# Kernel tuning notes

Hardware: AMD Instinct MI355X
Metric: run time of the kernel (lower is better)

The kernel has to match this reference:

```python
import jax, jax.numpy as jnp
import numpy as np

B, S, D, H = 2, 2048, 1024, 16
DK = D // H


def setup_inputs() -> dict:
    key = jax.random.key(0)
    ks = jax.random.split(key, 12)
    sc = 1.0 / np.sqrt(D)
    return {
        "q": jax.random.normal(ks[0], (B, S, D), jnp.float32),
        "k": jax.random.normal(ks[1], (B, S, D), jnp.float32),
        "v": jax.random.normal(ks[2], (B, S, D), jnp.float32),
        "mask": jax.random.randint(ks[3], (B, S), 0, 2, jnp.int32),
        "Wq": jax.random.normal(ks[4], (D, D), jnp.float32) * sc,
        "bq": jnp.zeros((D,), jnp.float32),
        "Wk": jax.random.normal(ks[5], (D, D), jnp.float32) * sc,
        "bk": jnp.zeros((D,), jnp.float32),
        "Wv": jax.random.normal(ks[6], (D, D), jnp.float32) * sc,
        "bv": jnp.zeros((D,), jnp.float32),
        "Wo": jax.random.normal(ks[7], (D, D), jnp.float32) * sc,
        "bo": jnp.zeros((D,), jnp.float32),
    }


def reference(q, k, v, mask, Wq, bq, Wk, bk, Wv, bv, Wo, bo):
    # Projections (flax nn.Dense: x @ W + b)
    query = q @ Wq + bq          # [B,S,D]
    key_ = k @ Wk + bk
    value = v @ Wv + bv
    # split heads -> [B,H,S,DK]
    def split(x):
        return x.reshape(B, S, H, DK).transpose(0, 2, 1, 3)
    qh, kh, vh = split(query), split(key_), split(value)
    scores = jnp.einsum('bhqd,bhkd->bhqk', qh, kh) / jnp.sqrt(jnp.float32(DK))
    # Faithful to source: mask=(mask==0); where(mask==0, -1e10, scores)
    # i.e. positions where ORIGINAL mask != 0 are set to -1e10.
    m = (mask == 0)[:, None, None, :]          # [B,1,1,S] bool
    scores = jnp.where(~m, jnp.float32(-1e10), scores)
    attn = jax.nn.softmax(scores, axis=-1)     # dropout deterministic (eval)
    x = jnp.einsum('bhqk,bhkd->bhqd', attn, vh)
    x = x.transpose(0, 2, 1, 3).reshape(B, S, D)
    return x @ Wo + bo
```

## Files before the change

kernel.cpp:

```cpp
#include <hip/hip_runtime.h>
#include <hip/hip_bf16.h>

typedef unsigned short u16;
typedef unsigned int u32;
typedef __attribute__((ext_vector_type(8))) __bf16 bf16x8;
typedef __attribute__((ext_vector_type(4))) float f32x4;
typedef __attribute__((ext_vector_type(16))) float f32x16;

constexpr int Bz = 2, Sq = 2048, Dm = 1024, Hn = 16, DK = 64;

__device__ __forceinline__ u16 f2bf(float f) {
    u32 u = __builtin_bit_cast(u32, f);
    return (u16)((u + 0x7FFFu + ((u >> 16) & 1u)) >> 16);
}

__device__ __forceinline__ u32 pack_bf16(float a, float b) {
#if __has_builtin(__builtin_amdgcn_cvt_pk_bf16_f32)
    return __builtin_bit_cast(u32, __builtin_amdgcn_cvt_pk_bf16_f32(a, b));
#else
    return (u32)f2bf(a) | ((u32)f2bf(b) << 16);
#endif
}

__device__ __forceinline__ bf16x8 lds_frag(const u16* p) {
    return __builtin_bit_cast(bf16x8, *(const uint4*)p);
}
__device__ __forceinline__ bf16x8 gfrag(const u16* p) {
    return __builtin_bit_cast(bf16x8, *(const uint4*)p);
}
__device__ __forceinline__ int swz(int r) { return (r ^ (r >> 3)) & 7; }

__device__ __forceinline__ void gll16(const u16* g, u16* l) {
    __builtin_amdgcn_global_load_lds(
        (const __attribute__((address_space(1))) void*)g,
        (__attribute__((address_space(3))) void*)l, 16, 0, 0);
}

__global__ __launch_bounds__(256) void mha_prep(
    const float* __restrict__ q, const float* __restrict__ k,
    const float* __restrict__ v,
    const float* __restrict__ w0, const float* __restrict__ w1,
    const float* __restrict__ w2, const float* __restrict__ w3,
    const int* __restrict__ mask,
    u16* __restrict__ qkv_dst, u16* __restrict__ wt_dst,
    float* __restrict__ biasg)
{
    __shared__ float tl[64 * 65];
    const int z = blockIdx.z, tid = threadIdx.x;
    if (z < 3) {
        const float* s = (z == 0) ? q : (z == 1) ? k : v;
        u16* d = qkv_dst + (size_t)z * 4 * 1024 * 1024;
        size_t i = ((size_t)blockIdx.x * 256 + tid) * 8;
        float4 a = *(const float4*)(s + i);
        float4 b = *(const float4*)(s + i + 4);
        *(uint4*)(d + i) = make_uint4(pack_bf16(a.x, a.y), pack_bf16(a.z, a.w),
                                      pack_bf16(b.x, b.y), pack_bf16(b.z, b.w));
        return;
    }
    const int bx = blockIdx.x;
    if (bx > 1024) return;
    if (bx == 1024) {
#pragma unroll
        for (int u = 0; u < 4; u++) {
            int4 mm = ((const int4*)mask)[tid * 4 + u];
            float4 bb;
            bb.x = mm.x ? -1.44269504e10f : 0.f;
            bb.y = mm.y ? -1.44269504e10f : 0.f;
            bb.z = mm.z ? -1.44269504e10f : 0.f;
            bb.w = mm.w ? -1.44269504e10f : 0.f;
            ((float4*)biasg)[tid * 4 + u] = bb;
        }
        return;
    }
    const int zi = bx >> 8, t = bx & 255, tr = t >> 4, tc = t & 15;
    const float* src = (zi == 0) ? w0 : (zi == 1) ? w1 : (zi == 2) ? w2 : w3;
    u16* d = wt_dst + (size_t)zi * Dm * Dm;
    {
        int r = tid >> 2, cq = (tid & 3) * 16;
        const float* sp = src + (size_t)(tr * 64 + r) * Dm + tc * 64 + cq;
#pragma unroll
        for (int j = 0; j < 4; j++) {
            float4 vv = *(const float4*)(sp + j * 4);
            tl[r * 65 + cq + j * 4 + 0] = vv.x;
            tl[r * 65 + cq + j * 4 + 1] = vv.y;
            tl[r * 65 + cq + j * 4 + 2] = vv.z;
            tl[r * 65 + cq + j * 4 + 3] = vv.w;
        }
    }
    __syncthreads();
    {
        int rr = tid >> 2, cc = (tid & 3) * 16;
        u16* dp = d + (size_t)(tc * 64 + rr) * Dm + tr * 64 + cc;
        u32 px[8];
#pragma unroll
        for (int j = 0; j < 8; j++)
            px[j] = pack_bf16(tl[(cc + 2 * j) * 65 + rr], tl[(cc + 2 * j + 1) * 65 + rr]);
        *(uint4*)dp       = make_uint4(px[0], px[1], px[2], px[3]);
        *(uint4*)(dp + 8) = make_uint4(px[4], px[5], px[6], px[7]);
    }
}

__device__ __forceinline__ void gemm_core_12864(
    const u16* __restrict__ Ab, const u16* __restrict__ Bb,
    u16* As, u16* Bs, f32x4 (&acc)[4][2])
{
    const int tid = threadIdx.x, lane = tid & 63;
    const int wm = (tid >> 7) & 1, wn = (tid >> 6) & 1;
    const int frow = lane & 15, quad = lane >> 4;

#pragma unroll
    for (int mi = 0; mi < 4; mi++)
#pragma unroll
        for (int ni = 0; ni < 2; ni++) acc[mi][ni] = (f32x4){0.f, 0.f, 0.f, 0.f};

    for (int k0 = 0; k0 < 1024; k0 += 64) {
#pragma unroll
        for (int i = 0; i < 4; i++) {
            int id = tid + i * 256, r = id >> 3, c = id & 7;
            gll16(Ab + (size_t)r * 1024 + k0 + (c ^ swz(r)) * 8, As + (size_t)id * 8);
        }
#pragma unroll
        for (int i = 0; i < 2; i++) {
            int id = tid + i * 256, r = id >> 3, c = id & 7;
            gll16(Bb + (size_t)r * 1024 + k0 + (c ^ swz(r)) * 8, Bs + (size_t)id * 8);
        }
        __syncthreads();
#pragma unroll
        for (int ks = 0; ks < 2; ks++) {
            bf16x8 af[4], bfr[2];
#pragma unroll
            for (int mi = 0; mi < 4; mi++) {
                int r = wm * 64 + mi * 16 + frow;
                af[mi] = lds_frag(As + r * 64 + ((ks * 4 + quad) ^ swz(r)) * 8);
            }
#pragma unroll
            for (int ni = 0; ni < 2; ni++) {
                int r = wn * 32 + ni * 16 + frow;
                bfr[ni] = lds_frag(Bs + r * 64 + ((ks * 4 + quad) ^ swz(r)) * 8);
            }
#pragma unroll
            for (int mi = 0; mi < 4; mi++)
#pragma unroll
                for (int ni = 0; ni < 2; ni++)
                    acc[mi][ni] = __builtin_amdgcn_mfma_f32_16x16x32_bf16(
                        af[mi], bfr[ni], acc[mi][ni], 0, 0, 0);
        }
        __syncthreads();
    }
}

__global__ __launch_bounds__(256) void mha_proj_qkv(
    const u16* __restrict__ Qb, const u16* __restrict__ Kb, const u16* __restrict__ Vb,
    const u16* __restrict__ Wqt, const u16* __restrict__ Wkt, const u16* __restrict__ Wvt,
    const float* __restrict__ bq, const float* __restrict__ bk, const float* __restrict__ bv,
    u16* __restrict__ Qh, u16* __restrict__ Kh, u16* __restrict__ Vt)
{
    __shared__ __align__(16) u16 As[128 * 64];
    __shared__ __align__(16) u16 Bs[64 * 64];
    const int z = blockIdx.z, bx = blockIdx.x;
    const u16* Ab; const u16* Bb; const float* bias;
    int m0, n0;
    if (z < 2) {
        m0 = (bx & 31) * 128;
        n0 = (bx >> 5) * 64;
        Ab = ((z == 0) ? Qb : Kb) + (size_t)m0 * Dm;
        Bb = ((z == 0) ? Wqt : Wkt) + (size_t)n0 * Dm;
        bias = (z == 0) ? bq : bk;
    } else {
        m0 = (bx >> 6) * 128;
        n0 = (bx & 63) * 64;
        Ab = Wvt + (size_t)m0 * Dm;
        Bb = Vb + (size_t)n0 * Dm;
        bias = bv;
    }

    f32x4 acc[4][2];
    gemm_core_12864(Ab, Bb, As, Bs, acc);

    const int tid = threadIdx.x, lane = tid & 63;
    const int wm = (tid >> 7) & 1, wn = (tid >> 6) & 1;
    const int frow = lane & 15, quad = lane >> 4;
    u16* dstq = (z == 0) ? Qh : Kh;
#pragma unroll
    for (int mi = 0; mi < 4; mi++)
#pragma unroll
        for (int ni = 0; ni < 2; ni++)
#pragma unroll
            for (int r = 0; r < 4; r++) {
                int i = m0 + wm * 64 + mi * 16 + quad * 4 + r;
                int j = n0 + wn * 32 + ni * 16 + frow;
                if (z < 2) {
                    float val = acc[mi][ni][r] + bias[j];
                    int b = i >> 11, s = i & (Sq - 1);
                    int h = j >> 6, dk = j & (DK - 1);
                    dstq[((size_t)(b * Hn + h) * Sq + s) * DK + dk] = f2bf(val);
                } else {
                    float val = acc[mi][ni][r] + bias[i];
                    int h = i >> 6, dk = i & (DK - 1);
                    int b = j >> 11, s = j & (Sq - 1);
                    int sp = (s & ~12) | ((s & 4) << 1) | ((s & 8) >> 1);
                    Vt[((size_t)(b * Hn + h) * DK + dk) * Sq + sp] = f2bf(val);
                }
            }
}

__global__ __launch_bounds__(512, 4) void mha_attn(
    const u16* __restrict__ Qh, const u16* __restrict__ Kh, const u16* __restrict__ Vt,
    const float* __restrict__ biasg, u16* __restrict__ X)
{
    const int bh = blockIdx.x;
    const int b = bh >> 4;
    const int q0 = blockIdx.y * 64;
    const int tid = threadIdx.x, lane = tid & 63, w = tid >> 6;
    const int wq = w & 1, p = w >> 1;
    const int qc = lane & 31, half = lane >> 5;
    constexpr float C2 = 0.125f * 1.44269504f;

    __shared__ __align__(16) u16 Ks[256 * 64];
    __shared__ __align__(16) u16 Vs[64 * 256];
    __shared__ float lsl[128];

    const u16* Qp = Qh + (size_t)bh * Sq * DK;
    const u16* Kp = Kh + (size_t)bh * Sq * DK;
    const u16* Vp = Vt + (size_t)bh * DK * Sq;
    const float* bp = biasg + b * Sq;

    bf16x8 qf[4];
    {
        const u16* qrow = Qp + (size_t)(q0 + wq * 32 + qc) * DK + half * 8;
#pragma unroll
        for (int kc = 0; kc < 4; kc++) qf[kc] = gfrag(qrow + kc * 16);
    }

    float l_l = 0.f;
    f32x16 o0, o1;
#pragma unroll
    for (int i = 0; i < 16; i++) { o0[i] = 0.f; o1[i] = 0.f; }

    for (int it = 0; it < 8; it++) {
        const int kb = it * 256;
#pragma unroll
        for (int i = 0; i < 4; i++) {
            int id = tid + i * 512;
            int kr = id >> 3, kc_ = id & 7;
            gll16(Kp + (size_t)(kb + kr) * DK + (kc_ ^ swz(kr)) * 8, Ks + (size_t)id * 8);
            int vr = id >> 5, vc = id & 31;
            gll16(Vp + (size_t)vr * Sq + kb + ((vc ^ (vr & 31)) * 8), Vs + (size_t)id * 8);
        }
        __syncthreads();

#pragma unroll
        for (int s = 0; s < 2; s++) {
            const int kr = p * 64 + s * 32 + qc;
            const int K0 = kb + p * 64 + s * 32;
            f32x16 sT;
#pragma unroll
            for (int i = 0; i < 16; i++) sT[i] = 0.f;
#pragma unroll
            for (int kc = 0; kc < 4; kc++) {
                bf16x8 ka = lds_frag(Ks + kr * 64 + ((kc * 2 + half) ^ swz(kr)) * 8);
                sT = __builtin_amdgcn_mfma_f32_32x32x16_bf16(ka, qf[kc], sT, 0, 0, 0);
            }

            float t[16], rs = 0.f;
#pragma unroll
            for (int g = 0; g < 4; g++) {
                float4 mb = *(const float4*)(bp + K0 + 8 * g + 4 * half);
#pragma unroll
                for (int r = 0; r < 4; r++) {
                    float bb = (r == 0) ? mb.x : (r == 1) ? mb.y : (r == 2) ? mb.z : mb.w;
                    float a = __builtin_amdgcn_exp2f(fmaf(sT[g * 4 + r], C2, bb));
                    t[g * 4 + r] = a; rs += a;
                }
            }
            l_l += rs;

            u32 pk[8];
#pragma unroll
            for (int i = 0; i < 8; i++) pk[i] = pack_bf16(t[2 * i], t[2 * i + 1]);

#pragma unroll
            for (int kc = 0; kc < 2; kc++) {
                bf16x8 pf = __builtin_bit_cast(bf16x8,
                    make_uint4(pk[4 * kc], pk[4 * kc + 1], pk[4 * kc + 2], pk[4 * kc + 3]));
                int ch = p * 8 + s * 4 + kc * 2 + half;
                bf16x8 va0 = lds_frag(Vs + qc * 256 + ((ch ^ (qc & 31)) * 8));
                bf16x8 va1 = lds_frag(Vs + (32 + qc) * 256 + ((ch ^ ((32 + qc) & 31)) * 8));
                o0 = __builtin_amdgcn_mfma_f32_32x32x16_bf16(va0, pf, o0, 0, 0, 0);
                o1 = __builtin_amdgcn_mfma_f32_32x32x16_bf16(va1, pf, o1, 0, 0, 0);
            }
        }
        __syncthreads();
    }

    l_l += __shfl_xor(l_l, 32);
    float* fc = (float*)Ks + wq * 2048;
#pragma unroll 1
    for (int src = 1; src < 4; src++) {
        if (p == src) {
#pragma unroll
            for (int r = 0; r < 16; r++) fc[r * 64 + lane] = o0[r];
#pragma unroll
            for (int r = 0; r < 16; r++) fc[(16 + r) * 64 + lane] = o1[r];
            lsl[wq * 64 + lane] = l_l;
        }
        __syncthreads();
        if (p == 0) {
#pragma unroll
            for (int r = 0; r < 16; r++) o0[r] += fc[r * 64 + lane];
#pragma unroll
            for (int r = 0; r < 16; r++) o1[r] += fc[(16 + r) * 64 + lane];
            l_l += lsl[wq * 64 + lane];
        }
        __syncthreads();
    }
    if (p == 0) {
        float inv = 1.0f / l_l;
        const int qg = q0 + wq * 32 + qc;
        u16* Xp = X + (size_t)(b * Sq + qg) * Dm + (bh & 15) * DK;
#pragma unroll
        for (int g = 0; g < 4; g++) {
            *(uint2*)&Xp[8 * g + 4 * half] =
                make_uint2(pack_bf16(o0[g * 4 + 0] * inv, o0[g * 4 + 1] * inv),
                           pack_bf16(o0[g * 4 + 2] * inv, o0[g * 4 + 3] * inv));
            *(uint2*)&Xp[32 + 8 * g + 4 * half] =
                make_uint2(pack_bf16(o1[g * 4 + 0] * inv, o1[g * 4 + 1] * inv),
                           pack_bf16(o1[g * 4 + 2] * inv, o1[g * 4 + 3] * inv));
        }
    }
}

__global__ __launch_bounds__(256) void mha_oproj(
    const u16* __restrict__ X, const u16* __restrict__ Wot,
    const float* __restrict__ bo, float* __restrict__ out)
{
    __shared__ __align__(16) u16 As[128 * 64];
    __shared__ __align__(16) u16 Bs[64 * 64];
    const int bx = blockIdx.x;
    const int m0 = (bx & 31) * 128, n0 = (bx >> 5) * 64;
    f32x4 acc[4][2];
    gemm_core_12864(X + (size_t)m0 * Dm, Wot + (size_t)n0 * Dm, As, Bs, acc);
    const int tid = threadIdx.x, lane = tid & 63;
    const int wm = (tid >> 7) & 1, wn = (tid >> 6) & 1;
    const int frow = lane & 15, quad = lane >> 4;
#pragma unroll
    for (int mi = 0; mi < 4; mi++)
#pragma unroll
        for (int ni = 0; ni < 2; ni++)
#pragma unroll
            for (int r = 0; r < 4; r++) {
                int m = m0 + wm * 64 + mi * 16 + quad * 4 + r;
                int n = n0 + wn * 32 + ni * 16 + frow;
                out[(size_t)m * Dm + n] = acc[mi][ni][r] + bo[n];
            }
}

extern "C" void kernel_launch(void* const* d_in, const int* in_sizes, int n_in,
                              void* d_out, int out_size, void* d_ws, size_t ws_size,
                              hipStream_t stream)
{
    const float* qin  = (const float*)d_in[0];
    const float* kin  = (const float*)d_in[1];
    const float* vin  = (const float*)d_in[2];
    const int*   mask = (const int*)d_in[3];
    const float* Wq   = (const float*)d_in[4];
    const float* bq   = (const float*)d_in[5];
    const float* Wk   = (const float*)d_in[6];
    const float* bk   = (const float*)d_in[7];
    const float* Wv   = (const float*)d_in[8];
    const float* bv   = (const float*)d_in[9];
    const float* Wo   = (const float*)d_in[10];
    const float* bo   = (const float*)d_in[11];
    float* out = (float*)d_out;

    u16* ws = (u16*)d_ws;
    const size_t MW = (size_t)Dm * Dm;
    const size_t MT = (size_t)Bz * Sq * Dm;
    u16* Wqt = ws;
    u16* Wkt = ws + MW;
    u16* Wvt = ws + 2 * MW;
    u16* Wot = ws + 3 * MW;
    u16* Qb  = ws + 4 * MW;
    u16* Kb  = Qb + MT;
    u16* Vb  = Kb + MT;
    u16* Qh  = Vb + MT;
    u16* Kh  = Qh + MT;
    u16* Vt  = Kh + MT;
    float* biasg = (float*)(Vt + MT);
    u16* X   = Qb;

    hipLaunchKernelGGL(mha_prep, dim3(2048, 1, 4), dim3(256), 0, stream,
                       qin, kin, vin, Wq, Wk, Wv, Wo, mask, Qb, Wqt, biasg);
    hipLaunchKernelGGL(mha_proj_qkv, dim3(512, 1, 3), dim3(256), 0, stream,
                       Qb, Kb, Vb, Wqt, Wkt, Wvt, bq, bk, bv, Qh, Kh, Vt);
    hipLaunchKernelGGL(mha_attn, dim3(32, 32), dim3(512), 0, stream,
                       Qh, Kh, Vt, biasg, X);
    hipLaunchKernelGGL(mha_oproj, dim3(512), dim3(256), 0, stream,
                       X, Wot, bo, out);
}
```

Before: 247.7 us.

## Compact unmasked keys and skip fully masked key tiles in attention

The prep kernel now prefix-scans the mask per batch. It builds a permutation that moves unmasked keys to the front, reorders the additive bias to match, and records the count of unmasked keys. The QKV projection writes K rows and V columns into that compacted order, so attention only loops over ceil(nk/128) key tiles instead of all 2048. Masked keys would only add exp of a huge negative number, so their work can be skipped. The attention loop also switches to double-buffered 128-key tiles with prefetch and setprio hints, and replaces the serial cross-wave output reduction with a two-level tree. Costs are scattered writes in the projection epilogue and an unhandled edge case when every key is masked (nk=0 leaves the row sum at zero).

```diff
diff --git a/kernel.cpp b/kernel.cpp
--- a/kernel.cpp
+++ b/kernel.cpp
@@ -43,9 +43,10 @@
     const float* __restrict__ w2, const float* __restrict__ w3,
     const int* __restrict__ mask,
     u16* __restrict__ qkv_dst, u16* __restrict__ wt_dst,
-    float* __restrict__ biasg)
+    float* __restrict__ biasg, int* __restrict__ compg, int* __restrict__ nkg)
 {
     __shared__ float tl[64 * 65];
+    __shared__ int sc[256];
     const int z = blockIdx.z, tid = threadIdx.x;
     if (z < 3) {
         const float* s = (z == 0) ? q : (z == 1) ? k : v;
@@ -58,18 +59,40 @@
         return;
     }
     const int bx = blockIdx.x;
-    if (bx > 1024) return;
-    if (bx == 1024) {
-#pragma unroll
-        for (int u = 0; u < 4; u++) {
-            int4 mm = ((const int4*)mask)[tid * 4 + u];
-            float4 bb;
-            bb.x = mm.x ? -1.44269504e10f : 0.f;
-            bb.y = mm.y ? -1.44269504e10f : 0.f;
-            bb.z = mm.z ? -1.44269504e10f : 0.f;
-            bb.w = mm.w ? -1.44269504e10f : 0.f;
-            ((float4*)biasg)[tid * 4 + u] = bb;
-        }
+    if (bx >= 1026) return;
+    if (bx >= 1024) {
+        const int b = bx - 1024;
+        const int* mp = mask + b * Sq;
+        int4 m0_ = ((const int4*)mp)[tid * 2];
+        int4 m1_ = ((const int4*)mp)[tid * 2 + 1];
+        int a[8];
+        a[0] = (m0_.x == 0); a[1] = (m0_.y == 0); a[2] = (m0_.z == 0); a[3] = (m0_.w == 0);
+        a[4] = (m1_.x == 0); a[5] = (m1_.y == 0); a[6] = (m1_.z == 0); a[7] = (m1_.w == 0);
+        int cnt = 0;
+#pragma unroll
+        for (int j = 0; j < 8; j++) cnt += a[j];
+        sc[tid] = cnt;
+        __syncthreads();
+        for (int off = 1; off < 256; off <<= 1) {
+            int u = (tid >= off) ? sc[tid - off] : 0;
+            int vv = sc[tid];
+            __syncthreads();
+            sc[tid] = vv + u;
+            __syncthreads();
+        }
+        const int incl = sc[tid];
+        const int nk = sc[255];
+        int pa = incl - cnt;
+        int pi = nk + tid * 8 - pa;
+        int* cp = compg + b * Sq;
+        float* bbp = biasg + b * Sq;
+#pragma unroll
+        for (int j = 0; j < 8; j++) {
+            int pos = a[j] ? pa++ : pi++;
+            cp[tid * 8 + j] = pos;
+            bbp[pos] = a[j] ? 0.f : -1.44269504e10f;
+        }
+        if (tid == 0) nkg[b] = nk;
         return;
     }
     const int zi = bx >> 8, t = bx & 255, tr = t >> 4, tc = t & 15;
@@ -153,6 +176,7 @@
     const u16* __restrict__ Qb, const u16* __restrict__ Kb, const u16* __restrict__ Vb,
     const u16* __restrict__ Wqt, const u16* __restrict__ Wkt, const u16* __restrict__ Wvt,
     const float* __restrict__ bq, const float* __restrict__ bk, const float* __restrict__ bv,
+    const int* __restrict__ comp,
     u16* __restrict__ Qh, u16* __restrict__ Kh, u16* __restrict__ Vt)
 {
     __shared__ __align__(16) u16 As[128 * 64];
@@ -193,20 +217,23 @@
                     float val = acc[mi][ni][r] + bias[j];
                     int b = i >> 11, s = i & (Sq - 1);
                     int h = j >> 6, dk = j & (DK - 1);
-                    dstq[((size_t)(b * Hn + h) * Sq + s) * DK + dk] = f2bf(val);
+                    int srow = (z == 1) ? comp[b * Sq + s] : s;
+                    dstq[((size_t)(b * Hn + h) * Sq + srow) * DK + dk] = f2bf(val);
                 } else {
                     float val = acc[mi][ni][r] + bias[i];
                     int h = i >> 6, dk = i & (DK - 1);
-                    int b = j >> 11, s = j & (Sq - 1);
-                    int sp = (s & ~12) | ((s & 4) << 1) | ((s & 8) >> 1);
-                    Vt[((size_t)(b * Hn + h) * DK + dk) * Sq + sp] = f2bf(val);
+                    int bj = j >> 11, s = j & (Sq - 1);
+                    int cs = comp[bj * Sq + s];
+                    int sp = (cs & ~12) | ((cs & 4) << 1) | ((cs & 8) >> 1);
+                    Vt[((size_t)(bj * Hn + h) * DK + dk) * Sq + sp] = f2bf(val);
                 }
             }
 }
 
 __global__ __launch_bounds__(512, 4) void mha_attn(
     const u16* __restrict__ Qh, const u16* __restrict__ Kh, const u16* __restrict__ Vt,
-    const float* __restrict__ biasg, u16* __restrict__ X)
+    const float* __restrict__ biasg, const int* __restrict__ nkg,
+    u16* __restrict__ X)
 {
     const int bh = blockIdx.x;
     const int b = bh >> 4;
@@ -216,14 +243,16 @@
     const int qc = lane & 31, half = lane >> 5;
     constexpr float C2 = 0.125f * 1.44269504f;
 
-    __shared__ __align__(16) u16 Ks[256 * 64];
-    __shared__ __align__(16) u16 Vs[64 * 256];
-    __shared__ float lsl[128];
+    __shared__ __align__(16) u16 Ks[2][128 * 64];
+    __shared__ __align__(16) u16 Vs[2][64 * 128];
+    __shared__ float lsl[256];
 
     const u16* Qp = Qh + (size_t)bh * Sq * DK;
     const u16* Kp = Kh + (size_t)bh * Sq * DK;
     const u16* Vp = Vt + (size_t)bh * DK * Sq;
     const float* bp = biasg + b * Sq;
+    const int nk = nkg[b];
+    const int nt = (nk + 127) >> 7;
 
     bf16x8 qf[4];
     {
@@ -232,89 +261,131 @@
         for (int kc = 0; kc < 4; kc++) qf[kc] = gfrag(qrow + kc * 16);
     }
 
+    const int idA = tid, idB = tid + 512;
+    const u16* ksA = Kp + (size_t)(idA >> 3) * DK + ((idA & 7) ^ swz(idA >> 3)) * 8;
+    const u16* ksB = Kp + (size_t)(idB >> 3) * DK + ((idB & 7) ^ swz(idB >> 3)) * 8;
+    const u16* vsA = Vp + (size_t)(idA >> 4) * Sq + (((idA & 15) ^ ((idA >> 4) & 15)) * 8);
+    const u16* vsB = Vp + (size_t)(idB >> 4) * Sq + (((idB & 15) ^ ((idB >> 4) & 15)) * 8);
+    u16* kdA = &Ks[0][idA * 8];
+    u16* kdB = &Ks[0][idB * 8];
+    u16* vdA = &Vs[0][idA * 8];
+    u16* vdB = &Vs[0][idB * 8];
+
+    auto stage = [&](int cur, int kb) {
+        const int co = cur * (128 * 64);
+        gll16(ksA + (size_t)kb * DK, kdA + co);
+        gll16(ksB + (size_t)kb * DK, kdB + co);
+        gll16(vsA + kb, vdA + co);
+        gll16(vsB + kb, vdB + co);
+    };
+
+    const int kr = p * 32 + qc;
+    int kfo[4];
+#pragma unroll
+    for (int kc = 0; kc < 4; kc++)
+        kfo[kc] = kr * 64 + (((kc * 2 + half) ^ swz(kr)) * 8);
+    int vfo0[2], vfo1[2];
+#pragma unroll
+    for (int kc = 0; kc < 2; kc++) {
+        int ch = p * 4 + kc * 2 + half;
+        vfo0[kc] = qc * 128 + ((ch ^ (qc & 15)) * 8);
+        vfo1[kc] = (32 + qc) * 128 + ((ch ^ (qc & 15)) * 8);
+    }
+    const float* bpw = bp + p * 32 + 4 * half;
+
     float l_l = 0.f;
     f32x16 o0, o1;
 #pragma unroll
     for (int i = 0; i < 16; i++) { o0[i] = 0.f; o1[i] = 0.f; }
 
-    for (int it = 0; it < 8; it++) {
-        const int kb = it * 256;
-#pragma unroll
-        for (int i = 0; i < 4; i++) {
-            int id = tid + i * 512;
-            int kr = id >> 3, kc_ = id & 7;
-            gll16(Kp + (size_t)(kb + kr) * DK + (kc_ ^ swz(kr)) * 8, Ks + (size_t)id * 8);
-            int vr = id >> 5, vc = id & 31;
-            gll16(Vp + (size_t)vr * Sq + kb + ((vc ^ (vr & 31)) * 8), Vs + (size_t)id * 8);
-        }
+    stage(0, 0);
+    __syncthreads();
+
+    for (int it = 0; it < nt; it++) {
+        const int cur = it & 1;
+        if (it + 1 < nt) stage(cur ^ 1, (it + 1) * 128);
+
+        const u16* Kl = Ks[cur];
+        const u16* Vl = Vs[cur];
+
+        f32x16 sT;
+#pragma unroll
+        for (int i = 0; i < 16; i++) sT[i] = 0.f;
+        __builtin_amdgcn_s_setprio(1);
+#pragma unroll
+        for (int kc = 0; kc < 4; kc++) {
+            bf16x8 ka = lds_frag(Kl + kfo[kc]);
+            sT = __builtin_amdgcn_mfma_f32_32x32x16_bf16(ka, qf[kc], sT, 0, 0, 0);
+        }
+        __builtin_amdgcn_s_setprio(0);
+
+        const int kb = it * 128;
+        float t[16], rs = 0.f;
+#pragma unroll
+        for (int g = 0; g < 4; g++) {
+            float4 mb = *(const float4*)(bpw + kb + 8 * g);
+#pragma unroll
+            for (int r = 0; r < 4; r++) {
+                float bb = (r == 0) ? mb.x : (r == 1) ? mb.y : (r == 2) ? mb.z : mb.w;
+                float a = __builtin_amdgcn_exp2f(fmaf(sT[g * 4 + r], C2, bb));
+                t[g * 4 + r] = a; rs += a;
+            }
+        }
+        l_l += rs;
+
+        u32 pk[8];
+#pragma unroll
+        for (int i = 0; i < 8; i++) pk[i] = pack_bf16(t[2 * i], t[2 * i + 1]);
+
+        __builtin_amdgcn_s_setprio(1);
+#pragma unroll
+        for (int kc = 0; kc < 2; kc++) {
+            bf16x8 pf = __builtin_bit_cast(bf16x8,
+                make_uint4(pk[4 * kc], pk[4 * kc + 1], pk[4 * kc + 2], pk[4 * kc + 3]));
+            bf16x8 va0 = lds_frag(Vl + vfo0[kc]);
+            bf16x8 va1 = lds_frag(Vl + vfo1[kc]);
+            o0 = __builtin_amdgcn_mfma_f32_32x32x16_bf16(va0, pf, o0, 0, 0, 0);
+            o1 = __builtin_amdgcn_mfma_f32_32x32x16_bf16(va1, pf, o1, 0, 0, 0);
+        }
+        __builtin_amdgcn_s_setprio(0);
         __syncthreads();
-
-#pragma unroll
-        for (int s = 0; s < 2; s++) {
-            const int kr = p * 64 + s * 32 + qc;
-            const int K0 = kb + p * 64 + s * 32;
-            f32x16 sT;
-#pragma unroll
-            for (int i = 0; i < 16; i++) sT[i] = 0.f;
-#pragma unroll
-            for (int kc = 0; kc < 4; kc++) {
-                bf16x8 ka = lds_frag(Ks + kr * 64 + ((kc * 2 + half) ^ swz(kr)) * 8);
-                sT = __builtin_amdgcn_mfma_f32_32x32x16_bf16(ka, qf[kc], sT, 0, 0, 0);
-            }
-
-            float t[16], rs = 0.f;
-#pragma unroll
-            for (int g = 0; g < 4; g++) {
-                float4 mb = *(const float4*)(bp + K0 + 8 * g + 4 * half);
-#pragma unroll
-                for (int r = 0; r < 4; r++) {
-                    float bb = (r == 0) ? mb.x : (r == 1) ? mb.y : (r == 2) ? mb.z : mb.w;
-                    float a = __builtin_amdgcn_exp2f(fmaf(sT[g * 4 + r], C2, bb));
-                    t[g * 4 + r] = a; rs += a;
-                }
-            }
-            l_l += rs;
-
-            u32 pk[8];
-#pragma unroll
-            for (int i = 0; i < 8; i++) pk[i] = pack_bf16(t[2 * i], t[2 * i + 1]);
-
-#pragma unroll
-            for (int kc = 0; kc < 2; kc++) {
-                bf16x8 pf = __builtin_bit_cast(bf16x8,
-                    make_uint4(pk[4 * kc], pk[4 * kc + 1], pk[4 * kc + 2], pk[4 * kc + 3]));
-                int ch = p * 8 + s * 4 + kc * 2 + half;
-                bf16x8 va0 = lds_frag(Vs + qc * 256 + ((ch ^ (qc & 31)) * 8));
-                bf16x8 va1 = lds_frag(Vs + (32 + qc) * 256 + ((ch ^ ((32 + qc) & 31)) * 8));
-                o0 = __builtin_amdgcn_mfma_f32_32x32x16_bf16(va0, pf, o0, 0, 0, 0);
-                o1 = __builtin_amdgcn_mfma_f32_32x32x16_bf16(va1, pf, o1, 0, 0, 0);
-            }
-        }
-        __syncthreads();
     }
 
     l_l += __shfl_xor(l_l, 32);
-    float* fc = (float*)Ks + wq * 2048;
-#pragma unroll 1
-    for (int src = 1; src < 4; src++) {
-        if (p == src) {
-#pragma unroll
-            for (int r = 0; r < 16; r++) fc[r * 64 + lane] = o0[r];
-#pragma unroll
-            for (int r = 0; r < 16; r++) fc[(16 + r) * 64 + lane] = o1[r];
-            lsl[wq * 64 + lane] = l_l;
-        }
-        __syncthreads();
-        if (p == 0) {
-#pragma unroll
-            for (int r = 0; r < 16; r++) o0[r] += fc[r * 64 + lane];
-#pragma unroll
-            for (int r = 0; r < 16; r++) o1[r] += fc[(16 + r) * 64 + lane];
-            l_l += lsl[wq * 64 + lane];
-        }
-        __syncthreads();
-    }
+    float* fcb = (float*)Ks;
+    if (p >= 2) {
+        float* fc = fcb + (size_t)(wq * 2 + (p & 1)) * 2048;
+#pragma unroll
+        for (int r = 0; r < 16; r++) fc[r * 64 + lane] = o0[r];
+#pragma unroll
+        for (int r = 0; r < 16; r++) fc[(16 + r) * 64 + lane] = o1[r];
+        lsl[(wq * 2 + (p & 1)) * 64 + lane] = l_l;
+    }
+    __syncthreads();
+    if (p < 2) {
+        float* fc = fcb + (size_t)(wq * 2 + p) * 2048;
+#pragma unroll
+        for (int r = 0; r < 16; r++) o0[r] += fc[r * 64 + lane];
+#pragma unroll
+        for (int r = 0; r < 16; r++) o1[r] += fc[(16 + r) * 64 + lane];
+        l_l += lsl[(wq * 2 + p) * 64 + lane];
+    }
+    if (p == 1) {
+        float* fc = fcb + (size_t)(wq * 2 + 1) * 2048;
+#pragma unroll
+        for (int r = 0; r < 16; r++) fc[r * 64 + lane] = o0[r];
+#pragma unroll
+        for (int r = 0; r < 16; r++) fc[(16 + r) * 64 + lane] = o1[r];
+        lsl[(wq * 2 + 1) * 64 + lane] = l_l;
+    }
+    __syncthreads();
     if (p == 0) {
+        float* fc = fcb + (size_t)(wq * 2 + 1) * 2048;
+#pragma unroll
+        for (int r = 0; r < 16; r++) o0[r] += fc[r * 64 + lane];
+#pragma unroll
+        for (int r = 0; r < 16; r++) o1[r] += fc[(16 + r) * 64 + lane];
+        l_l += lsl[(wq * 2 + 1) * 64 + lane];
         float inv = 1.0f / l_l;
         const int qg = q0 + wq * 32 + qc;
         u16* Xp = X + (size_t)(b * Sq + qg) * Dm + (bh & 15) * DK;
@@ -387,14 +458,16 @@
     u16* Kh  = Qh + MT;
     u16* Vt  = Kh + MT;
     float* biasg = (float*)(Vt + MT);
+    int*   compg = (int*)(biasg + Bz * Sq);
+    int*   nkg   = (int*)(compg + Bz * Sq);
     u16* X   = Qb;
 
     hipLaunchKernelGGL(mha_prep, dim3(2048, 1, 4), dim3(256), 0, stream,
-                       qin, kin, vin, Wq, Wk, Wv, Wo, mask, Qb, Wqt, biasg);
+                       qin, kin, vin, Wq, Wk, Wv, Wo, mask, Qb, Wqt, biasg, compg, nkg);
     hipLaunchKernelGGL(mha_proj_qkv, dim3(512, 1, 3), dim3(256), 0, stream,
-                       Qb, Kb, Vb, Wqt, Wkt, Wvt, bq, bk, bv, Qh, Kh, Vt);
+                       Qb, Kb, Vb, Wqt, Wkt, Wvt, bq, bk, bv, compg, Qh, Kh, Vt);
     hipLaunchKernelGGL(mha_attn, dim3(32, 32), dim3(512), 0, stream,
-                       Qh, Kh, Vt, biasg, X);
+                       Qh, Kh, Vt, biasg, nkg, X);
     hipLaunchKernelGGL(mha_oproj, dim3(512), dim3(256), 0, stream,
                        X, Wot, bo, out);
 }
```

Measured after the change: 221.5 us. 1.12x faster.
